# Kernel tuning notes

Measured on AMD Instinct MI355X. Metric: run time of the kernel, lower is better.

The kernel has to match this reference:

```python
import jax, jax.numpy as jnp
import numpy as np

N_NODES = 100000
N_EDGES = 1600000
D_IN = 128
D_HID = 128
D_OUT = 128


def sage_conv(x, src, dst, W_l, b_l, W_r, n_nodes):
    # PyG SAGEConv (mean aggr): out = Linear_l(mean_j x_j) + Linear_r(x_i)
    msg = x[src]                                            # [E, d] gather
    agg = jax.ops.segment_sum(msg, dst, num_segments=n_nodes)  # [N, d]
    cnt = jax.ops.segment_sum(jnp.ones((src.shape[0],), x.dtype), dst,
                              num_segments=n_nodes)
    mean = agg / jnp.maximum(cnt, 1.0)[:, None]             # mean over neighbors
    return mean @ W_l.T + b_l + x @ W_r.T


def setup_inputs() -> dict:
    key = jax.random.key(0)
    ks = jax.random.split(key, 8)
    x = jax.random.normal(ks[0], (N_NODES, D_IN), dtype=jnp.float32)
    edge_index = jax.random.randint(ks[1], (2, N_EDGES), 0, N_NODES, dtype=jnp.int64)
    s1 = 1.0 / np.sqrt(D_IN)
    s2 = 1.0 / np.sqrt(D_HID)
    W1_l = jax.random.uniform(ks[2], (D_HID, D_IN), jnp.float32, -s1, s1)
    b1_l = jax.random.uniform(ks[3], (D_HID,), jnp.float32, -s1, s1)
    W1_r = jax.random.uniform(ks[4], (D_HID, D_IN), jnp.float32, -s1, s1)
    W2_l = jax.random.uniform(ks[5], (D_OUT, D_HID), jnp.float32, -s2, s2)
    b2_l = jax.random.uniform(ks[6], (D_OUT,), jnp.float32, -s2, s2)
    W2_r = jax.random.uniform(ks[7], (D_OUT, D_HID), jnp.float32, -s2, s2)
    return {"x": x, "edge_index": edge_index, "W1_l": W1_l, "b1_l": b1_l,
            "W1_r": W1_r, "W2_l": W2_l, "b2_l": b2_l, "W2_r": W2_r}


def reference(x, edge_index, W1_l, b1_l, W1_r, W2_l, b2_l, W2_r):
    src, dst = edge_index[0], edge_index[1]
    n = x.shape[0]
    h = sage_conv(x, src, dst, W1_l, b1_l, W1_r, n)
    h = jax.nn.relu(h)
    # F.dropout with training=False (eval mode) is identity
    out = sage_conv(h, src, dst, W2_l, b2_l, W2_r, n)
    return out
```

## Files before the change

### kernel.cpp

```cpp
#include <hip/hip_runtime.h>

typedef __attribute__((ext_vector_type(8))) short short8;
typedef __attribute__((ext_vector_type(4))) float f32x4;
typedef __attribute__((ext_vector_type(2))) float f32x2;

#define NBMAX 512
#define CAP 8192

__device__ inline unsigned short f2bf(float f) {
  union { float f; unsigned u; } v; v.f = f;
  unsigned r = v.u + 0x7fffu + ((v.u >> 16) & 1u);
  return (unsigned short)(r >> 16);
}

__device__ inline void addf2(f32x2 (&a)[4], uint4 v) {
  union { uint2 u; f32x2 f; } t;
  t.u.x = v.x << 16; t.u.y = v.x & 0xffff0000u; a[0] += t.f;
  t.u.x = v.y << 16; t.u.y = v.y & 0xffff0000u; a[1] += t.f;
  t.u.x = v.z << 16; t.u.y = v.z & 0xffff0000u; a[2] += t.f;
  t.u.x = v.w << 16; t.u.y = v.w & 0xffff0000u; a[3] += t.f;
}

__device__ inline int load_src(const int* ei, int E, int e, int f64) {
  return f64 ? ei[2 * e] : ei[e];
}
__device__ inline int load_dst(const int* ei, int E, int e, int f64) {
  return f64 ? ei[2 * (E + e)] : ei[E + e];
}

__global__ __launch_bounds__(256) void prep(
    const int* __restrict__ ei, int E,
    int* __restrict__ btot, int2* __restrict__ stage, int SB,
    const float* __restrict__ x, unsigned short* __restrict__ xb, int n8,
    const float* __restrict__ W1l, const float* __restrict__ W1r,
    const float* __restrict__ W2l, const float* __restrict__ W2r,
    unsigned short* __restrict__ Wp) {
  __shared__ int lcnt[NBMAX];
  __shared__ int lbase[NBMAX];
  __shared__ int sflag;
  const int b = blockIdx.x;
  const int t = threadIdx.x;

  if (b < SB) {
    if (t == 0) sflag = 0;
    for (int i = t; i < NBMAX; i += 256) lcnt[i] = 0;
    __syncthreads();
    const int e0 = b * 4096;
    {
      int e = e0 + t;
      int v = (e < E) ? ei[2 * e + 1] : 0;
      if (v) atomicOr(&sflag, 1);
    }
    __syncthreads();
    const int f64 = (sflag == 0) ? 1 : 0;

    int srcs[16], bks[16];
    int dsts[16];
#pragma unroll
    for (int i = 0; i < 16; ++i) {
      int e = e0 + i * 256 + t;
      if (e < E) {
        srcs[i] = load_src(ei, E, e, f64);
        int d = load_dst(ei, E, e, f64);
        dsts[i] = d;
        bks[i] = d >> 8;
        atomicAdd(&lcnt[d >> 8], 1);
      } else {
        bks[i] = -1;
      }
    }
    __syncthreads();
    for (int i = t; i < NBMAX; i += 256) {
      int c = lcnt[i];
      lbase[i] = c ? atomicAdd(&btot[i], c) : 0;
    }
    __syncthreads();
    for (int i = t; i < NBMAX; i += 256) lcnt[i] = 0;
    __syncthreads();
#pragma unroll
    for (int i = 0; i < 16; ++i) {
      int bk = bks[i];
      if (bk >= 0) {
        int r = atomicAdd(&lcnt[bk], 1);
        stage[(size_t)bk * CAP + lbase[bk] + r] = make_int2(srcs[i], dsts[i]);
      }
    }
    return;
  }

  if (b < SB + 4) {
    const int m = b - SB;
    const float* W = (m == 0) ? W1l : (m == 1) ? W1r : (m == 2) ? W2l : W2r;
    unsigned short* dst = Wp + (size_t)m * 16384;
#pragma unroll
    for (int it = 0; it < 8; ++it) {
      int id = it * 256 + t;
      int j = id >> 4;
      int kc = id & 15;
      int s = kc >> 2, q = kc & 3;
      int jt = j >> 4, nn2 = j & 15;
      int c = (s * 8 + jt) * 4 + q;
      const float* src = W + j * 128 + kc * 8;
      union { unsigned short u[8]; uint4 v; } tv;
#pragma unroll
      for (int k = 0; k < 8; ++k) tv.u[k] = f2bf(src[k]);
      *(uint4*)(dst + (c * 16 + nn2) * 8) = tv.v;
    }
    return;
  }

  const int cb = b - SB - 4;
  const int nxb = gridDim.x - SB - 4;
  int i = cb * 256 + t;
  const int stride = nxb * 256;
  for (; i < n8; i += stride) {
    float4 v0 = ((const float4*)x)[2 * i];
    float4 v1 = ((const float4*)x)[2 * i + 1];
    union { unsigned short u[8]; uint4 v; } tv;
    tv.u[0] = f2bf(v0.x); tv.u[1] = f2bf(v0.y);
    tv.u[2] = f2bf(v0.z); tv.u[3] = f2bf(v0.w);
    tv.u[4] = f2bf(v1.x); tv.u[5] = f2bf(v1.y);
    tv.u[6] = f2bf(v1.z); tv.u[7] = f2bf(v1.w);
    ((uint4*)xb)[i] = tv.v;
  }
}

__global__ __launch_bounds__(256) void bucket_fill2(
    const int2* __restrict__ stage, const int* __restrict__ btot,
    int* __restrict__ offs, int* __restrict__ cnt, float* __restrict__ inv,
    int* __restrict__ csr, int N) {
  __shared__ int lhist[256];
  __shared__ int lscan[256];
  __shared__ int lcur[256];
  __shared__ int red[256];
  const int b = blockIdx.x;
  const int t = threadIdx.x;
  int sum = 0;
  for (int j = t; j < b; j += 256) sum += btot[j];
  red[t] = sum;
  lhist[t] = 0;
  __syncthreads();
  for (int d = 128; d; d >>= 1) {
    if (t < d) red[t] += red[t + d];
    __syncthreads();
  }
  const int base = red[0];
  const int count = btot[b];
  const int2* sp = stage + (size_t)b * CAP;
  for (int i = t; i < count; i += 256)
    atomicAdd(&lhist[sp[i].y & 255], 1);
  __syncthreads();
  int v = lhist[t];
  lscan[t] = v;
  __syncthreads();
  for (int d = 1; d < 256; d <<= 1) {
    int tv = (t >= d) ? lscan[t - d] : 0;
    __syncthreads();
    lscan[t] += tv;
    __syncthreads();
  }
  const int excl = lscan[t] - v;
  const int node = b * 256 + t;
  if (node < N) {
    offs[node] = base + excl;
    cnt[node] = v;
    inv[node] = 1.0f / (float)((v > 1) ? v : 1);
  }
  lcur[t] = base + excl;
  __syncthreads();
  for (int i = t; i < count; i += 256) {
    int2 sd = sp[i];
    int p = atomicAdd(&lcur[sd.y & 255], 1);
    csr[p] = sd.x;
  }
}

template <int RELU, int OUTBF>
__global__ __launch_bounds__(256, 4) void agg_gemm(
    const unsigned short* __restrict__ A,
    const unsigned short* __restrict__ Wp,
    const float* __restrict__ bias, const float* __restrict__ inv,
    const int* __restrict__ offs, const int* __restrict__ cnt,
    const int* __restrict__ csr, void* __restrict__ outp, int n) {
  __shared__ unsigned short wsh[16384];
  const int tid = threadIdx.x;

  {
    const uint4* wsrc = (const uint4*)Wp;
    uint4* wdst = (uint4*)wsh;
#pragma unroll
    for (int it = 0; it < 8; ++it) wdst[it * 256 + tid] = wsrc[it * 256 + tid];
  }

  const int lane = tid & 63;
  const int wave = tid >> 6;
  const int nn = lane & 15;
  const int quad = lane >> 4;
  const int rowbase = blockIdx.x * 64 + wave * 16;

  int nodeA = rowbase + nn;
  if (nodeA > n - 1) nodeA = n - 1;

  short8 asf[4];
#pragma unroll
  for (int s = 0; s < 4; ++s)
    asf[s] = *(const short8*)(A + (size_t)nodeA * 128 + s * 32 + quad * 8);

  const int deg = cnt[nodeA];
  const int off0 = offs[nodeA];
  const float sc = inv[nodeA];

  int md = deg;
  md = max(md, __shfl_xor(md, 1));
  md = max(md, __shfl_xor(md, 2));
  md = max(md, __shfl_xor(md, 4));
  md = max(md, __shfl_xor(md, 8));

  f32x2 acc[4][4];
#pragma unroll
  for (int s = 0; s < 4; ++s)
#pragma unroll
    for (int p = 0; p < 4; ++p) acc[s][p] = (f32x2){0.f, 0.f};

  const char* Abase = (const char*)A;
  const int qoff = quad * 16;

  int i0 = (0 < deg) ? csr[off0] : 0;
  int i1 = (1 < deg) ? csr[off0 + 1] : 0;
  for (int j = 0; j < md; j += 2) {
    int ni0 = (j + 2 < deg) ? csr[off0 + j + 2] : 0;
    int ni1 = (j + 3 < deg) ? csr[off0 + j + 3] : 0;
    const char* p0 = Abase + ((size_t)(unsigned)i0 << 8) + qoff;
    const char* p1 = Abase + ((size_t)(unsigned)i1 << 8) + qoff;
    uint4 v0[4], v1[4];
#pragma unroll
    for (int s = 0; s < 4; ++s) v0[s] = *(const uint4*)(p0 + s * 64);
#pragma unroll
    for (int s = 0; s < 4; ++s) v1[s] = *(const uint4*)(p1 + s * 64);
    if (j < deg) {
#pragma unroll
      for (int s = 0; s < 4; ++s) addf2(acc[s], v0[s]);
    }
    if (j + 1 < deg) {
#pragma unroll
      for (int s = 0; s < 4; ++s) addf2(acc[s], v1[s]);
    }
    i0 = ni0; i1 = ni1;
  }

  short8 am[4];
#pragma unroll
  for (int s = 0; s < 4; ++s) {
    union { unsigned short u[8]; short8 v; } t;
#pragma unroll
    for (int p = 0; p < 4; ++p) {
      t.u[2 * p] = f2bf(acc[s][p].x * sc);
      t.u[2 * p + 1] = f2bf(acc[s][p].y * sc);
    }
    am[s] = t.v;
  }

  f32x4 accc[8];
#pragma unroll
  for (int jt = 0; jt < 8; ++jt) accc[jt] = (f32x4){0.f, 0.f, 0.f, 0.f};

  __syncthreads();

#pragma unroll
  for (int jt = 0; jt < 8; ++jt) {
#pragma unroll
    for (int s = 0; s < 4; ++s) {
      int c = (s * 8 + jt) * 4 + quad;
      short8 bl = *(const short8*)(wsh + (c * 16 + nn) * 8);
      accc[jt] = __builtin_amdgcn_mfma_f32_16x16x32_bf16(am[s], bl, accc[jt], 0, 0, 0);
    }
  }

  __syncthreads();

  {
    const uint4* wsrc = (const uint4*)(Wp + 16384);
    uint4* wdst = (uint4*)wsh;
#pragma unroll
    for (int it = 0; it < 8; ++it) wdst[it * 256 + tid] = wsrc[it * 256 + tid];
  }
  __syncthreads();

#pragma unroll
  for (int jt = 0; jt < 8; ++jt) {
#pragma unroll
    for (int s = 0; s < 4; ++s) {
      int c = (s * 8 + jt) * 4 + quad;
      short8 br = *(const short8*)(wsh + (c * 16 + nn) * 8);
      accc[jt] = __builtin_amdgcn_mfma_f32_16x16x32_bf16(asf[s], br, accc[jt], 0, 0, 0);
    }
  }

#pragma unroll
  for (int jt = 0; jt < 8; ++jt) {
    int col = jt * 16 + nn;
    float bv = bias[col];
#pragma unroll
    for (int r = 0; r < 4; ++r) {
      int ro = rowbase + quad * 4 + r;
      if (ro < n) {
        float o = accc[jt][r] + bv;
        if (RELU) o = fmaxf(o, 0.f);
        if (OUTBF) {
          ((unsigned short*)outp)[(size_t)ro * 128 + col] = f2bf(o);
        } else {
          ((float*)outp)[(size_t)ro * 128 + col] = o;
        }
      }
    }
  }
}


extern "C" void kernel_launch(void* const* d_in, const int* in_sizes, int n_in,
                              void* d_out, int out_size, void* d_ws, size_t ws_size,
                              hipStream_t stream) {
  const float* x = (const float*)d_in[0];
  const int* ei = (const int*)d_in[1];
  const float* W1l = (const float*)d_in[2];
  const float* b1 = (const float*)d_in[3];
  const float* W1r = (const float*)d_in[4];
  const float* W2l = (const float*)d_in[5];
  const float* b2 = (const float*)d_in[6];
  const float* W2r = (const float*)d_in[7];
  float* out = (float*)d_out;

  const int N = in_sizes[0] / 128;
  const int E = in_sizes[1] / 2;
  const int nb = (N + 255) / 256;

  char* p = (char*)d_ws;
  auto alloc = [&](size_t bytes) {
    char* r = p;
    p += (bytes + 255) & ~(size_t)255;
    return r;
  };
  int* btot = (int*)alloc((size_t)NBMAX * 4);
  int* cnt = (int*)alloc((size_t)N * 4);
  int* offs = (int*)alloc((size_t)N * 4);
  float* inv = (float*)alloc((size_t)N * 4);
  int* csr = (int*)alloc((size_t)E * 4);
  unsigned short* Wpb = (unsigned short*)alloc((size_t)4 * 16384 * 2);
  size_t stage_bytes = (size_t)nb * CAP * 8;
  size_t hb_bytes = (size_t)N * 128 * 2;
  char* shared_region = alloc(stage_bytes > hb_bytes ? stage_bytes : hb_bytes);
  unsigned short* hb = (unsigned short*)shared_region;
  int2* stage = (int2*)shared_region;

  unsigned short* xb = (unsigned short*)d_out;

  hipMemsetAsync(btot, 0, (size_t)nb * 4, stream);

  const int SB = (E + 4095) / 4096;
  prep<<<SB + 4 + 2048, 256, 0, stream>>>(ei, E, btot, stage, SB,
                                          x, xb, N * 128 / 8,
                                          W1l, W1r, W2l, W2r, Wpb);
  bucket_fill2<<<nb, 256, 0, stream>>>(stage, btot, offs, cnt, inv, csr, N);

  const int gb = (N + 63) / 64;

  agg_gemm<1, 1><<<gb, 256, 0, stream>>>(xb, Wpb, b1, inv, offs, cnt, csr,
                                         (void*)hb, N);
  agg_gemm<0, 0><<<gb, 256, 0, stream>>>(hb, Wpb + 32768, b2, inv, offs, cnt, csr,
                                         (void*)out, N);
}
```

Baseline: 329.4 us.

## Make agg_gemm persistent with both weight matrices resident in LDS

The aggregation+GEMM kernel becomes a grid-stride persistent kernel with 512 blocks. Each block loads both W_l and W_r into 64KB of shared memory once, so the per-chunk weight reload and the extra barriers go away. The neighbor gather loop is unrolled to four edges per iteration to keep more loads in flight. The cost is higher LDS use and a launch bound of 2 blocks per CU, which lowers occupancy for a latency-bound gather.

```diff
diff --git a/kernel.cpp b/kernel.cpp
--- a/kernel.cpp
+++ b/kernel.cpp
@@ -176,140 +176,126 @@
 }
 
 template <int RELU, int OUTBF>
-__global__ __launch_bounds__(256, 4) void agg_gemm(
+__global__ __launch_bounds__(256, 2) void agg_gemm(
     const unsigned short* __restrict__ A,
     const unsigned short* __restrict__ Wp,
     const float* __restrict__ bias, const float* __restrict__ inv,
     const int* __restrict__ offs, const int* __restrict__ cnt,
-    const int* __restrict__ csr, void* __restrict__ outp, int n) {
-  __shared__ unsigned short wsh[16384];
+    const int* __restrict__ csr, void* __restrict__ outp, int n, int nchunks) {
+  __shared__ unsigned short wsh[2 * 16384];
   const int tid = threadIdx.x;
 
   {
     const uint4* wsrc = (const uint4*)Wp;
     uint4* wdst = (uint4*)wsh;
 #pragma unroll
-    for (int it = 0; it < 8; ++it) wdst[it * 256 + tid] = wsrc[it * 256 + tid];
-  }
+    for (int it = 0; it < 16; ++it) wdst[it * 256 + tid] = wsrc[it * 256 + tid];
+  }
+  __syncthreads();
 
   const int lane = tid & 63;
   const int wave = tid >> 6;
   const int nn = lane & 15;
   const int quad = lane >> 4;
-  const int rowbase = blockIdx.x * 64 + wave * 16;
-
-  int nodeA = rowbase + nn;
-  if (nodeA > n - 1) nodeA = n - 1;
-
-  short8 asf[4];
-#pragma unroll
-  for (int s = 0; s < 4; ++s)
-    asf[s] = *(const short8*)(A + (size_t)nodeA * 128 + s * 32 + quad * 8);
-
-  const int deg = cnt[nodeA];
-  const int off0 = offs[nodeA];
-  const float sc = inv[nodeA];
-
-  int md = deg;
-  md = max(md, __shfl_xor(md, 1));
-  md = max(md, __shfl_xor(md, 2));
-  md = max(md, __shfl_xor(md, 4));
-  md = max(md, __shfl_xor(md, 8));
-
-  f32x2 acc[4][4];
-#pragma unroll
-  for (int s = 0; s < 4; ++s)
-#pragma unroll
-    for (int p = 0; p < 4; ++p) acc[s][p] = (f32x2){0.f, 0.f};
-
+  const int qoff = quad * 16;
   const char* Abase = (const char*)A;
-  const int qoff = quad * 16;
-
-  int i0 = (0 < deg) ? csr[off0] : 0;
-  int i1 = (1 < deg) ? csr[off0 + 1] : 0;
-  for (int j = 0; j < md; j += 2) {
-    int ni0 = (j + 2 < deg) ? csr[off0 + j + 2] : 0;
-    int ni1 = (j + 3 < deg) ? csr[off0 + j + 3] : 0;
-    const char* p0 = Abase + ((size_t)(unsigned)i0 << 8) + qoff;
-    const char* p1 = Abase + ((size_t)(unsigned)i1 << 8) + qoff;
-    uint4 v0[4], v1[4];
-#pragma unroll
-    for (int s = 0; s < 4; ++s) v0[s] = *(const uint4*)(p0 + s * 64);
-#pragma unroll
-    for (int s = 0; s < 4; ++s) v1[s] = *(const uint4*)(p1 + s * 64);
-    if (j < deg) {
-#pragma unroll
-      for (int s = 0; s < 4; ++s) addf2(acc[s], v0[s]);
-    }
-    if (j + 1 < deg) {
-#pragma unroll
-      for (int s = 0; s < 4; ++s) addf2(acc[s], v1[s]);
-    }
-    i0 = ni0; i1 = ni1;
-  }
-
-  short8 am[4];
-#pragma unroll
-  for (int s = 0; s < 4; ++s) {
-    union { unsigned short u[8]; short8 v; } t;
-#pragma unroll
-    for (int p = 0; p < 4; ++p) {
-      t.u[2 * p] = f2bf(acc[s][p].x * sc);
-      t.u[2 * p + 1] = f2bf(acc[s][p].y * sc);
-    }
-    am[s] = t.v;
-  }
-
-  f32x4 accc[8];
-#pragma unroll
-  for (int jt = 0; jt < 8; ++jt) accc[jt] = (f32x4){0.f, 0.f, 0.f, 0.f};
-
-  __syncthreads();
-
-#pragma unroll
-  for (int jt = 0; jt < 8; ++jt) {
+
+  for (int ch = blockIdx.x; ch < nchunks; ch += gridDim.x) {
+    const int rowbase = ch * 64 + wave * 16;
+    int nodeA = rowbase + nn;
+    if (nodeA > n - 1) nodeA = n - 1;
+
+    short8 asf[4];
+#pragma unroll
+    for (int s = 0; s < 4; ++s)
+      asf[s] = *(const short8*)(A + (size_t)nodeA * 128 + s * 32 + quad * 8);
+
+    const int deg = cnt[nodeA];
+    const int off0 = offs[nodeA];
+    const float sc = inv[nodeA];
+
+    int md = deg;
+    md = max(md, __shfl_xor(md, 1));
+    md = max(md, __shfl_xor(md, 2));
+    md = max(md, __shfl_xor(md, 4));
+    md = max(md, __shfl_xor(md, 8));
+
+    f32x2 acc[4][4];
+#pragma unroll
+    for (int s = 0; s < 4; ++s)
+#pragma unroll
+      for (int p = 0; p < 4; ++p) acc[s][p] = (f32x2){0.f, 0.f};
+
+    int idx[4];
+#pragma unroll
+    for (int u = 0; u < 4; ++u) idx[u] = (u < deg) ? csr[off0 + u] : 0;
+
+    for (int j = 0; j < md; j += 4) {
+      int nidx[4];
+#pragma unroll
+      for (int u = 0; u < 4; ++u)
+        nidx[u] = (j + 4 + u < deg) ? csr[off0 + j + 4 + u] : 0;
+      uint4 v[4][4];
+#pragma unroll
+      for (int u = 0; u < 4; ++u) {
+        const char* pp = Abase + ((size_t)(unsigned)idx[u] << 8) + qoff;
+#pragma unroll
+        for (int s = 0; s < 4; ++s) v[u][s] = *(const uint4*)(pp + s * 64);
+      }
+#pragma unroll
+      for (int u = 0; u < 4; ++u) {
+        if (j + u < deg) {
+#pragma unroll
+          for (int s = 0; s < 4; ++s) addf2(acc[s], v[u][s]);
+        }
+      }
+#pragma unroll
+      for (int u = 0; u < 4; ++u) idx[u] = nidx[u];
+    }
+
+    short8 am[4];
 #pragma unroll
     for (int s = 0; s < 4; ++s) {
-      int c = (s * 8 + jt) * 4 + quad;
-      short8 bl = *(const short8*)(wsh + (c * 16 + nn) * 8);
-      accc[jt] = __builtin_amdgcn_mfma_f32_16x16x32_bf16(am[s], bl, accc[jt], 0, 0, 0);
-    }
-  }
-
-  __syncthreads();
-
-  {
-    const uint4* wsrc = (const uint4*)(Wp + 16384);
-    uint4* wdst = (uint4*)wsh;
-#pragma unroll
-    for (int it = 0; it < 8; ++it) wdst[it * 256 + tid] = wsrc[it * 256 + tid];
-  }
-  __syncthreads();
-
-#pragma unroll
-  for (int jt = 0; jt < 8; ++jt) {
-#pragma unroll
-    for (int s = 0; s < 4; ++s) {
-      int c = (s * 8 + jt) * 4 + quad;
-      short8 br = *(const short8*)(wsh + (c * 16 + nn) * 8);
-      accc[jt] = __builtin_amdgcn_mfma_f32_16x16x32_bf16(asf[s], br, accc[jt], 0, 0, 0);
-    }
-  }
-
-#pragma unroll
-  for (int jt = 0; jt < 8; ++jt) {
-    int col = jt * 16 + nn;
-    float bv = bias[col];
-#pragma unroll
-    for (int r = 0; r < 4; ++r) {
-      int ro = rowbase + quad * 4 + r;
-      if (ro < n) {
-        float o = accc[jt][r] + bv;
-        if (RELU) o = fmaxf(o, 0.f);
-        if (OUTBF) {
-          ((unsigned short*)outp)[(size_t)ro * 128 + col] = f2bf(o);
-        } else {
-          ((float*)outp)[(size_t)ro * 128 + col] = o;
+      union { unsigned short u[8]; short8 v; } t;
+#pragma unroll
+      for (int p = 0; p < 4; ++p) {
+        t.u[2 * p] = f2bf(acc[s][p].x * sc);
+        t.u[2 * p + 1] = f2bf(acc[s][p].y * sc);
+      }
+      am[s] = t.v;
+    }
+
+    f32x4 accc[8];
+#pragma unroll
+    for (int jt = 0; jt < 8; ++jt) accc[jt] = (f32x4){0.f, 0.f, 0.f, 0.f};
+
+#pragma unroll
+    for (int jt = 0; jt < 8; ++jt) {
+#pragma unroll
+      for (int s = 0; s < 4; ++s) {
+        int c = (s * 8 + jt) * 4 + quad;
+        short8 bl = *(const short8*)(wsh + (c * 16 + nn) * 8);
+        short8 br = *(const short8*)(wsh + 16384 + (c * 16 + nn) * 8);
+        accc[jt] = __builtin_amdgcn_mfma_f32_16x16x32_bf16(am[s], bl, accc[jt], 0, 0, 0);
+        accc[jt] = __builtin_amdgcn_mfma_f32_16x16x32_bf16(asf[s], br, accc[jt], 0, 0, 0);
+      }
+    }
+
+#pragma unroll
+    for (int jt = 0; jt < 8; ++jt) {
+      int col = jt * 16 + nn;
+      float bv = bias[col];
+#pragma unroll
+      for (int r = 0; r < 4; ++r) {
+        int ro = rowbase + quad * 4 + r;
+        if (ro < n) {
+          float o = accc[jt][r] + bv;
+          if (RELU) o = fmaxf(o, 0.f);
+          if (OUTBF) {
+            ((unsigned short*)outp)[(size_t)ro * 128 + col] = f2bf(o);
+          } else {
+            ((float*)outp)[(size_t)ro * 128 + col] = o;
+          }
         }
       }
     }
@@ -363,9 +349,10 @@
   bucket_fill2<<<nb, 256, 0, stream>>>(stage, btot, offs, cnt, inv, csr, N);
 
   const int gb = (N + 63) / 64;
-
-  agg_gemm<1, 1><<<gb, 256, 0, stream>>>(xb, Wpb, b1, inv, offs, cnt, csr,
-                                         (void*)hb, N);
-  agg_gemm<0, 0><<<gb, 256, 0, stream>>>(hb, Wpb + 32768, b2, inv, offs, cnt, csr,
-                                         (void*)out, N);
-}
+  const int PB = gb < 512 ? gb : 512;
+
+  agg_gemm<1, 1><<<PB, 256, 0, stream>>>(xb, Wpb, b1, inv, offs, cnt, csr,
+                                         (void*)hb, N, gb);
+  agg_gemm<0, 0><<<PB, 256, 0, stream>>>(hb, Wpb + 32768, b2, inv, offs, cnt, csr,
+                                         (void*)out, N, gb);
+}
```

Result: slower. 419.9 us (+27.5%).
